# Kernel tuning notes

Measured on AMD Instinct MI355X. Metric: run time of the kernel, lower is better.

Reference implementation:

```python
import jax, jax.numpy as jnp
import numpy as np

TOP_K = 4
ALPHA = 1.702
LIMIT = 7.0


def _glu(x):
    # interleaved gate/up split, clamp, custom swiglu
    gate = x[..., ::2]
    up = x[..., 1::2]
    gate = jnp.minimum(gate, LIMIT)
    up = jnp.clip(up, -LIMIT, LIMIT)
    glu = gate * jax.nn.sigmoid(gate * ALPHA)
    return (up + 1.0) * glu


def setup_inputs() -> dict:
    key = jax.random.key(0)
    ks = jax.random.split(key, 7)
    B, S, H, F, E = 1, 1024, 2880, 2880, 16
    w_scale = 0.02
    return {
        "hidden_states": jax.random.normal(ks[0], (B, S, H), dtype=jnp.float32),
        "router_w": jax.random.normal(ks[1], (E, H), dtype=jnp.float32) * w_scale,
        "router_b": jax.random.normal(ks[2], (E,), dtype=jnp.float32) * w_scale,
        "gate_up_w": jax.random.normal(ks[3], (E, H, 2 * F), dtype=jnp.float32) * w_scale,
        "gate_up_b": jax.random.normal(ks[4], (E, 2 * F), dtype=jnp.float32) * w_scale,
        "down_w": jax.random.normal(ks[5], (E, F, H), dtype=jnp.float32) * w_scale,
        "down_b": jax.random.normal(ks[6], (E, H), dtype=jnp.float32) * w_scale,
    }


def reference(hidden_states, router_w, router_b, gate_up_w, gate_up_b, down_w, down_b):
    B, S, H = hidden_states.shape
    x = hidden_states.reshape(-1, H)  # [T, H]
    T = x.shape[0]

    # Router: linear + top-k + softmax over top-k values, scattered to full [T, E]
    logits = x @ router_w.T + router_b  # [T, E]
    top_v, top_i = jax.lax.top_k(logits, TOP_K)  # [T, K]
    top_v = jax.nn.softmax(top_v, axis=-1)  # normalized top-k affinities
    scores = jnp.zeros_like(logits).at[jnp.arange(T)[:, None], top_i].set(top_v)  # [T, E]

    # Expert GLU MLPs (dense over experts; zero affinity masks unselected experts)
    gu = jnp.einsum('th,ehf->etf', x, gate_up_w) + gate_up_b[:, None, :]  # [E, T, 2F]
    act = _glu(gu)  # [E, T, F]
    out_e = jnp.einsum('etf,efh->eth', act, down_w) + down_b[:, None, :]  # [E, T, H]

    # Combine weighted by router scores
    out = jnp.einsum('te,eth->th', scores, out_e)  # [T, H]
    return out.reshape(B, S, H)
```

## Files before the change

### kernel.cpp

```cpp
#include <hip/hip_runtime.h>
#include <hip/hip_bf16.h>
#include <math.h>

#define H_DIM 2880
#define F_DIM 2880
#define GU_DIM 5760
#define NE 16
#define NT 1024
#define TOPK 4

typedef float f32x4 __attribute__((ext_vector_type(4)));
typedef __bf16 bf16x8 __attribute__((ext_vector_type(8)));

__device__ __forceinline__ unsigned short f2bf(float f) {
    union { float f; unsigned u; } v; v.f = f;
    return (unsigned short)((v.u + 0x8000u) >> 16);
}
__device__ __forceinline__ unsigned pk2(float a, float b) {
    return (unsigned)f2bf(a) | ((unsigned)f2bf(b) << 16);
}
__device__ __forceinline__ void gload16(const void* gsrc, void* ldst) {
    __builtin_amdgcn_global_load_lds(
        (const __attribute__((address_space(1))) unsigned int*)gsrc,
        (__attribute__((address_space(3))) unsigned int*)ldst,
        16, 0, 0);
}

__global__ __launch_bounds__(256) void castx_kernel(const float* __restrict__ x,
                                                    unsigned short* __restrict__ xb)
{
    int i = (blockIdx.x * 256 + threadIdx.x) * 8;
    float4 a = *(const float4*)(x + i);
    float4 b = *(const float4*)(x + i + 4);
    uint4 o;
    o.x = pk2(a.x, a.y); o.y = pk2(a.z, a.w);
    o.z = pk2(b.x, b.y); o.w = pk2(b.z, b.w);
    *(uint4*)(xb + i) = o;
}

__global__ __launch_bounds__(64) void router_kernel(
    const float* __restrict__ x, const float* __restrict__ rw, const float* __restrict__ rb,
    int* counts, int* topk_idx, float* topk_score)
{
    int t = blockIdx.x, lane = threadIdx.x;
    const float* xr = x + (size_t)t * H_DIM;
    float acc[NE];
#pragma unroll
    for (int e = 0; e < NE; e++) acc[e] = 0.f;
    for (int h = lane; h < H_DIM; h += 64) {
        float xv = xr[h];
#pragma unroll
        for (int e = 0; e < NE; e++) acc[e] += xv * rw[e * H_DIM + h];
    }
    float lg[NE];
#pragma unroll
    for (int e = 0; e < NE; e++) {
        float v = acc[e];
#pragma unroll
        for (int off = 32; off > 0; off >>= 1) v += __shfl_down(v, off, 64);
        lg[e] = v;
    }
    if (lane == 0) {
#pragma unroll
        for (int e = 0; e < NE; e++) lg[e] += rb[e];
        int mask = 0; float tv[TOPK]; int ti[TOPK];
        for (int k = 0; k < TOPK; k++) {
            float best = -1e30f; int bi = 0;
            for (int e = 0; e < NE; e++)
                if (!((mask >> e) & 1) && lg[e] > best) { best = lg[e]; bi = e; }
            mask |= 1 << bi; tv[k] = best; ti[k] = bi;
        }
        float m = tv[0], s = 0.f, ex[TOPK];
        for (int k = 0; k < TOPK; k++) { ex[k] = expf(tv[k] - m); s += ex[k]; }
        float inv = 1.f / s;
        for (int k = 0; k < TOPK; k++) {
            topk_idx[t * TOPK + k] = ti[k];
            topk_score[t * TOPK + k] = ex[k] * inv;
            atomicAdd(&counts[ti[k]], 1);
        }
    }
}

__global__ void offsets_kernel(const int* counts, int* offsets) {
    if (threadIdx.x == 0 && blockIdx.x == 0) {
        int s = 0;
        for (int e = 0; e < NE; e++) { offsets[e] = s; s += counts[e]; }
        offsets[NE] = s;
    }
}

__global__ void scatter_kernel(const int* topk_idx, const float* topk_score,
                               const int* offsets, int* fills, int* entry, float* entry_score,
                               int* slot_map)
{
    int t = blockIdx.x * blockDim.x + threadIdx.x;
    if (t >= NT) return;
    for (int k = 0; k < TOPK; k++) {
        int e = topk_idx[t * TOPK + k];
        int pos = atomicAdd(&fills[e], 1);
        int i = offsets[e] + pos;
        entry[i] = t | (k << 16);
        entry_score[i] = topk_score[t * TOPK + k];
        slot_map[t * TOPK + k] = i;
    }
}

__global__ __launch_bounds__(256, 2) void gemm1_kernel(
    const unsigned short* __restrict__ xb, const float* __restrict__ gw, const float* __restrict__ gb,
    const int* __restrict__ counts, const int* __restrict__ offsets,
    const int* __restrict__ entry, unsigned short* __restrict__ act)
{
    int e = blockIdx.z;
    int cnt = counts[e];
    int m0 = blockIdx.y * 128;
    if (m0 >= cnt) return;
    int n0 = blockIdx.x * 128;
    int off = offsets[e];

    __shared__ __align__(16) unsigned short As[128 * 32];
    __shared__ __align__(16) unsigned short Bs[128 * 40];
    __shared__ int toks[128];

    int tid = threadIdx.x;
    if (tid < 128) {
        int r = m0 + tid;
        toks[tid] = entry[off + (r < cnt ? r : 0)] & 0xFFFF;
    }
    __syncthreads();

    int wv = tid >> 6, lane = tid & 63;

    int ar0 = 32 * wv + (lane >> 2);
    int ar1 = ar0 + 16;
    int ac = lane & 3;
    const unsigned short* asrc0 = xb + (size_t)toks[ar0] * H_DIM + 8 * (ac ^ ((ar0 >> 1) & 3));
    const unsigned short* asrc1 = xb + (size_t)toks[ar1] * H_DIM + 8 * (ac ^ ((ar1 >> 1) & 3));
    unsigned short* adst0 = &As[(32 * wv) * 32];
    unsigned short* adst1 = &As[(32 * wv + 16) * 32];

    int n4 = tid & 31, kb = tid >> 5;
    const float* bptr = gw + (size_t)e * H_DIM * GU_DIM + (size_t)kb * 4 * GU_DIM + n0 + n4 * 4;

    int wm = (wv & 1) * 64, wn = (wv >> 1) * 64;
    int r16 = lane & 15, q = lane >> 4;

    f32x4 acc[4][4] = {};
    int a_rd[4], b_rd[4];
#pragma unroll
    for (int i = 0; i < 4; i++) {
        int m = wm + i * 16 + r16;
        a_rd[i] = m * 32 + ((q ^ ((m >> 1) & 3)) * 8);
        int n = wn + i * 16 + r16;
        b_rd[i] = n * 40 + ((q ^ ((n >> 2) & 3)) * 8);
    }
    int bwr[4];
#pragma unroll
    for (int c = 0; c < 4; c++) {
        int nl = n4 * 4 + c;
        bwr[c] = nl * 40 + (((kb >> 1) ^ ((nl >> 2) & 3)) * 8) + (kb & 1) * 4;
    }

    for (int k0 = 0; k0 < H_DIM; k0 += 32) {
        gload16(asrc0 + k0, adst0);
        gload16(asrc1 + k0, adst1);
        float bvf[4][4];
#pragma unroll
        for (int j = 0; j < 4; j++) {
            float4 tv = *(const float4*)(bptr + (size_t)(k0 + j) * GU_DIM);
            bvf[j][0] = tv.x; bvf[j][1] = tv.y; bvf[j][2] = tv.z; bvf[j][3] = tv.w;
        }
#pragma unroll
        for (int c = 0; c < 4; c++)
            *(uint2*)&Bs[bwr[c]] = make_uint2(pk2(bvf[0][c], bvf[1][c]), pk2(bvf[2][c], bvf[3][c]));
        __syncthreads();

        bf16x8 af[4], bq[4];
#pragma unroll
        for (int i = 0; i < 4; i++) af[i] = *(const bf16x8*)&As[a_rd[i]];
#pragma unroll
        for (int i = 0; i < 4; i++) bq[i] = *(const bf16x8*)&Bs[b_rd[i]];
#pragma unroll
        for (int mi = 0; mi < 4; mi++)
#pragma unroll
            for (int ni = 0; ni < 4; ni++)
                acc[mi][ni] = __builtin_amdgcn_mfma_f32_16x16x32_bf16(af[mi], bq[ni], acc[mi][ni], 0, 0, 0);
        __syncthreads();
    }

    const float* gbp = gb + (size_t)e * GU_DIM;
#pragma unroll
    for (int ni = 0; ni < 4; ni++) {
        int col = n0 + wn + ni * 16 + r16;
        float bias = gbp[col];
#pragma unroll
        for (int mi = 0; mi < 4; mi++) {
#pragma unroll
            for (int r = 0; r < 4; r++) {
                float v = acc[mi][ni][r] + bias;
                float vo = __shfl_xor(v, 1, 64);
                float gate = (lane & 1) ? vo : v;
                float up   = (lane & 1) ? v  : vo;
                gate = fminf(gate, 7.0f);
                up = fminf(fmaxf(up, -7.0f), 7.0f);
                float glu = gate / (1.0f + expf(-1.702f * gate));
                float a = (up + 1.0f) * glu;
                int row = m0 + wm + mi * 16 + q * 4 + r;
                if (row < cnt && !(lane & 1))
                    act[(size_t)(off + row) * F_DIM + (col >> 1)] = f2bf(a);
            }
        }
    }
}

__global__ __launch_bounds__(256, 2) void gemm2_kernel(
    const unsigned short* __restrict__ act, const float* __restrict__ dw, const float* __restrict__ db,
    const int* __restrict__ counts, const int* __restrict__ offsets,
    const float* __restrict__ entry_score, float* __restrict__ slot_out)
{
    int e = blockIdx.z;
    int cnt = counts[e];
    int m0 = blockIdx.y * 128;
    if (m0 >= cnt) return;
    int n0 = blockIdx.x * 128;
    int off = offsets[e];

    __shared__ __align__(16) unsigned short As[128 * 32];
    __shared__ __align__(16) unsigned short Bs[128 * 40];
    __shared__ float scs[128];

    int tid = threadIdx.x;
    if (tid < 128) {
        int r = m0 + tid;
        scs[tid] = entry_score[off + (r < cnt ? r : 0)];
    }
    __syncthreads();

    int wv = tid >> 6, lane = tid & 63;

    int ar0 = 32 * wv + (lane >> 2);
    int ar1 = ar0 + 16;
    int ac = lane & 3;
    const unsigned short* asrc0 = act + (size_t)(off + m0 + ar0) * F_DIM + 8 * (ac ^ ((ar0 >> 1) & 3));
    const unsigned short* asrc1 = act + (size_t)(off + m0 + ar1) * F_DIM + 8 * (ac ^ ((ar1 >> 1) & 3));
    unsigned short* adst0 = &As[(32 * wv) * 32];
    unsigned short* adst1 = &As[(32 * wv + 16) * 32];

    int n4 = tid & 31, kb = tid >> 5;
    int ncol = n0 + n4 * 4;
    bool nval = ncol < H_DIM;
    const float* bptr = dw + (size_t)e * F_DIM * H_DIM + (size_t)kb * 4 * H_DIM + ncol;

    int wm = (wv & 1) * 64, wn = (wv >> 1) * 64;
    int r16 = lane & 15, q = lane >> 4;

    f32x4 acc[4][4] = {};
    int a_rd[4], b_rd[4];
#pragma unroll
    for (int i = 0; i < 4; i++) {
        int m = wm + i * 16 + r16;
        a_rd[i] = m * 32 + ((q ^ ((m >> 1) & 3)) * 8);
        int n = wn + i * 16 + r16;
        b_rd[i] = n * 40 + ((q ^ ((n >> 2) & 3)) * 8);
    }
    int bwr[4];
#pragma unroll
    for (int c = 0; c < 4; c++) {
        int nl = n4 * 4 + c;
        bwr[c] = nl * 40 + (((kb >> 1) ^ ((nl >> 2) & 3)) * 8) + (kb & 1) * 4;
    }

    for (int k0 = 0; k0 < F_DIM; k0 += 32) {
        gload16(asrc0 + k0, adst0);
        gload16(asrc1 + k0, adst1);
        float bvf[4][4];
#pragma unroll
        for (int j = 0; j < 4; j++) {
            float4 tv = nval ? *(const float4*)(bptr + (size_t)(k0 + j) * H_DIM)
                             : make_float4(0.f, 0.f, 0.f, 0.f);
            bvf[j][0] = tv.x; bvf[j][1] = tv.y; bvf[j][2] = tv.z; bvf[j][3] = tv.w;
        }
#pragma unroll
        for (int c = 0; c < 4; c++)
            *(uint2*)&Bs[bwr[c]] = make_uint2(pk2(bvf[0][c], bvf[1][c]), pk2(bvf[2][c], bvf[3][c]));
        __syncthreads();

        bf16x8 af[4], bq[4];
#pragma unroll
        for (int i = 0; i < 4; i++) af[i] = *(const bf16x8*)&As[a_rd[i]];
#pragma unroll
        for (int i = 0; i < 4; i++) bq[i] = *(const bf16x8*)&Bs[b_rd[i]];
#pragma unroll
        for (int mi = 0; mi < 4; mi++)
#pragma unroll
            for (int ni = 0; ni < 4; ni++)
                acc[mi][ni] = __builtin_amdgcn_mfma_f32_16x16x32_bf16(af[mi], bq[ni], acc[mi][ni], 0, 0, 0);
        __syncthreads();
    }

    const float* dbp = db + (size_t)e * H_DIM;
#pragma unroll
    for (int ni = 0; ni < 4; ni++) {
        int col = n0 + wn + ni * 16 + r16;
        float bias = (col < H_DIM) ? dbp[col] : 0.f;
#pragma unroll
        for (int mi = 0; mi < 4; mi++) {
#pragma unroll
            for (int r = 0; r < 4; r++) {
                int lr = wm + mi * 16 + q * 4 + r;
                if (m0 + lr < cnt && col < H_DIM) {
                    float v = (acc[mi][ni][r] + bias) * scs[lr];
                    slot_out[(size_t)(off + m0 + lr) * H_DIM + col] = v;
                }
            }
        }
    }
}

__global__ __launch_bounds__(256) void gather_kernel(
    const float* __restrict__ slot_out, const int* __restrict__ slot_map,
    float* __restrict__ out)
{
    int t = blockIdx.x;
    int s0 = slot_map[t * TOPK + 0];
    int s1 = slot_map[t * TOPK + 1];
    int s2 = slot_map[t * TOPK + 2];
    int s3 = slot_map[t * TOPK + 3];
    const float* r0 = slot_out + (size_t)s0 * H_DIM;
    const float* r1 = slot_out + (size_t)s1 * H_DIM;
    const float* r2 = slot_out + (size_t)s2 * H_DIM;
    const float* r3 = slot_out + (size_t)s3 * H_DIM;
    float* op = out + (size_t)t * H_DIM;
    for (int h = threadIdx.x * 4; h < H_DIM; h += 1024) {
        f32x4 v = *(const f32x4*)(r0 + h) + *(const f32x4*)(r1 + h)
                + *(const f32x4*)(r2 + h) + *(const f32x4*)(r3 + h);
        *(f32x4*)(op + h) = v;
    }
}

extern "C" void kernel_launch(void* const* d_in, const int* in_sizes, int n_in,
                              void* d_out, int out_size, void* d_ws, size_t ws_size,
                              hipStream_t stream)
{
    const float* x  = (const float*)d_in[0];
    const float* rw = (const float*)d_in[1];
    const float* rb = (const float*)d_in[2];
    const float* gw = (const float*)d_in[3];
    const float* gb = (const float*)d_in[4];
    const float* dw = (const float*)d_in[5];
    const float* db = (const float*)d_in[6];
    float* out = (float*)d_out;

    char* ws = (char*)d_ws;
    int*   counts      = (int*)(ws);
    int*   fills       = (int*)(ws + 64);
    int*   offsets     = (int*)(ws + 128);
    int*   topk_idx    = (int*)(ws + 256);
    float* topk_score  = (float*)(ws + 16640);
    int*   entry       = (int*)(ws + 33024);
    float* entry_score = (float*)(ws + 49408);
    int*   slot_map    = (int*)(ws + 65792);
    unsigned short* act = (unsigned short*)(ws + 131072);
    unsigned short* xb  = (unsigned short*)(ws + 131072 + 24330240);
    float* slot_out     = (float*)(ws + 30359552);

    hipMemsetAsync(ws, 0, 256, stream);

    castx_kernel<<<1440, 256, 0, stream>>>(x, xb);
    router_kernel<<<NT, 64, 0, stream>>>(x, rw, rb, counts, topk_idx, topk_score);
    offsets_kernel<<<1, 32, 0, stream>>>(counts, offsets);
    scatter_kernel<<<4, 256, 0, stream>>>(topk_idx, topk_score, offsets, fills, entry, entry_score, slot_map);
    gemm1_kernel<<<dim3(45, 8, NE), 256, 0, stream>>>(xb, gw, gb, counts, offsets, entry, act);
    gemm2_kernel<<<dim3(23, 8, NE), 256, 0, stream>>>(act, dw, db, counts, offsets, entry_score, slot_out);
    gather_kernel<<<NT, 256, 0, stream>>>(slot_out, slot_map, out);
}
```

Before: 2.142 ms.

## Double-buffer LDS and enlarge M tile to 256 rows in expert GEMMs

Both expert GEMM kernels now use 512-thread blocks covering 256 token rows, so each converted fp32 weight tile is reused across twice as many rows. LDS is double-buffered: the next A tile and the next weight loads are issued before the current MFMA step, and the weight tile is stored after it, leaving one barrier per iteration. This targets the heavy fp32 weight traffic and load latency, at the cost of more LDS, padded work for experts with few tokens, and fewer blocks in the grid. Workspace offsets are shifted so the act buffer has room for the larger padded row reads.

```diff
diff --git a/kernel.cpp b/kernel.cpp
--- a/kernel.cpp
+++ b/kernel.cpp
@@ -8,6 +8,7 @@
 #define NE 16
 #define NT 1024
 #define TOPK 4
+#define NIT (H_DIM / 32)
 
 typedef float f32x4 __attribute__((ext_vector_type(4)));
 typedef __bf16 bf16x8 __attribute__((ext_vector_type(8)));
@@ -105,24 +106,24 @@
     }
 }
 
-__global__ __launch_bounds__(256, 2) void gemm1_kernel(
+__global__ __launch_bounds__(512) void gemm1_kernel(
     const unsigned short* __restrict__ xb, const float* __restrict__ gw, const float* __restrict__ gb,
     const int* __restrict__ counts, const int* __restrict__ offsets,
     const int* __restrict__ entry, unsigned short* __restrict__ act)
 {
     int e = blockIdx.z;
     int cnt = counts[e];
-    int m0 = blockIdx.y * 128;
+    int m0 = blockIdx.y * 256;
     if (m0 >= cnt) return;
     int n0 = blockIdx.x * 128;
     int off = offsets[e];
 
-    __shared__ __align__(16) unsigned short As[128 * 32];
-    __shared__ __align__(16) unsigned short Bs[128 * 40];
-    __shared__ int toks[128];
+    __shared__ __align__(16) unsigned short As[2][256 * 32];
+    __shared__ __align__(16) unsigned short Bs[2][128 * 40];
+    __shared__ int toks[256];
 
     int tid = threadIdx.x;
-    if (tid < 128) {
+    if (tid < 256) {
         int r = m0 + tid;
         toks[tid] = entry[off + (r < cnt ? r : 0)] & 0xFFFF;
     }
@@ -135,13 +136,19 @@
     int ac = lane & 3;
     const unsigned short* asrc0 = xb + (size_t)toks[ar0] * H_DIM + 8 * (ac ^ ((ar0 >> 1) & 3));
     const unsigned short* asrc1 = xb + (size_t)toks[ar1] * H_DIM + 8 * (ac ^ ((ar1 >> 1) & 3));
-    unsigned short* adst0 = &As[(32 * wv) * 32];
-    unsigned short* adst1 = &As[(32 * wv + 16) * 32];
-
-    int n4 = tid & 31, kb = tid >> 5;
+    int aoff0 = (32 * wv) * 32;
+    int aoff1 = (32 * wv + 16) * 32;
+
+    int n4 = tid & 31, kb = (tid >> 5) & 7;
     const float* bptr = gw + (size_t)e * H_DIM * GU_DIM + (size_t)kb * 4 * GU_DIM + n0 + n4 * 4;
-
-    int wm = (wv & 1) * 64, wn = (wv >> 1) * 64;
+    int bwr[4];
+#pragma unroll
+    for (int c = 0; c < 4; c++) {
+        int nl = n4 * 4 + c;
+        bwr[c] = nl * 40 + (((kb >> 1) ^ ((nl >> 2) & 3)) * 8) + (kb & 1) * 4;
+    }
+
+    int wm = (wv >> 1) * 64, wn = (wv & 1) * 64;
     int r16 = lane & 15, q = lane >> 4;
 
     f32x4 acc[4][4] = {};
@@ -153,37 +160,53 @@
         int n = wn + i * 16 + r16;
         b_rd[i] = n * 40 + ((q ^ ((n >> 2) & 3)) * 8);
     }
-    int bwr[4];
-#pragma unroll
-    for (int c = 0; c < 4; c++) {
-        int nl = n4 * 4 + c;
-        bwr[c] = nl * 40 + (((kb >> 1) ^ ((nl >> 2) & 3)) * 8) + (kb & 1) * 4;
-    }
-
-    for (int k0 = 0; k0 < H_DIM; k0 += 32) {
-        gload16(asrc0 + k0, adst0);
-        gload16(asrc1 + k0, adst1);
+
+    gload16(asrc0, &As[0][aoff0]);
+    gload16(asrc1, &As[0][aoff1]);
+    if (tid < 256) {
         float bvf[4][4];
 #pragma unroll
         for (int j = 0; j < 4; j++) {
-            float4 tv = *(const float4*)(bptr + (size_t)(k0 + j) * GU_DIM);
+            float4 tv = *(const float4*)(bptr + (size_t)j * GU_DIM);
             bvf[j][0] = tv.x; bvf[j][1] = tv.y; bvf[j][2] = tv.z; bvf[j][3] = tv.w;
         }
 #pragma unroll
         for (int c = 0; c < 4; c++)
-            *(uint2*)&Bs[bwr[c]] = make_uint2(pk2(bvf[0][c], bvf[1][c]), pk2(bvf[2][c], bvf[3][c]));
-        __syncthreads();
-
+            *(uint2*)&Bs[0][bwr[c]] = make_uint2(pk2(bvf[0][c], bvf[1][c]), pk2(bvf[2][c], bvf[3][c]));
+    }
+    __syncthreads();
+
+    for (int it = 0; it < NIT; it++) {
+        int cur = it & 1, nxt = cur ^ 1;
+        int k1 = (it + 1) * 32;
+        bool more = (it + 1 < NIT);
+        float bvf[4][4];
+        if (more) {
+            gload16(asrc0 + k1, &As[nxt][aoff0]);
+            gload16(asrc1 + k1, &As[nxt][aoff1]);
+            if (tid < 256) {
+#pragma unroll
+                for (int j = 0; j < 4; j++) {
+                    float4 tv = *(const float4*)(bptr + (size_t)(k1 + j) * GU_DIM);
+                    bvf[j][0] = tv.x; bvf[j][1] = tv.y; bvf[j][2] = tv.z; bvf[j][3] = tv.w;
+                }
+            }
+        }
         bf16x8 af[4], bq[4];
 #pragma unroll
-        for (int i = 0; i < 4; i++) af[i] = *(const bf16x8*)&As[a_rd[i]];
-#pragma unroll
-        for (int i = 0; i < 4; i++) bq[i] = *(const bf16x8*)&Bs[b_rd[i]];
+        for (int i = 0; i < 4; i++) af[i] = *(const bf16x8*)&As[cur][a_rd[i]];
+#pragma unroll
+        for (int i = 0; i < 4; i++) bq[i] = *(const bf16x8*)&Bs[cur][b_rd[i]];
 #pragma unroll
         for (int mi = 0; mi < 4; mi++)
 #pragma unroll
             for (int ni = 0; ni < 4; ni++)
                 acc[mi][ni] = __builtin_amdgcn_mfma_f32_16x16x32_bf16(af[mi], bq[ni], acc[mi][ni], 0, 0, 0);
+        if (more && tid < 256) {
+#pragma unroll
+            for (int c = 0; c < 4; c++)
+                *(uint2*)&Bs[nxt][bwr[c]] = make_uint2(pk2(bvf[0][c], bvf[1][c]), pk2(bvf[2][c], bvf[3][c]));
+        }
         __syncthreads();
     }
 
@@ -212,24 +235,24 @@
     }
 }
 
-__global__ __launch_bounds__(256, 2) void gemm2_kernel(
+__global__ __launch_bounds__(512) void gemm2_kernel(
     const unsigned short* __restrict__ act, const float* __restrict__ dw, const float* __restrict__ db,
     const int* __restrict__ counts, const int* __restrict__ offsets,
     const float* __restrict__ entry_score, float* __restrict__ slot_out)
 {
     int e = blockIdx.z;
     int cnt = counts[e];
-    int m0 = blockIdx.y * 128;
+    int m0 = blockIdx.y * 256;
     if (m0 >= cnt) return;
     int n0 = blockIdx.x * 128;
     int off = offsets[e];
 
-    __shared__ __align__(16) unsigned short As[128 * 32];
-    __shared__ __align__(16) unsigned short Bs[128 * 40];
-    __shared__ float scs[128];
+    __shared__ __align__(16) unsigned short As[2][256 * 32];
+    __shared__ __align__(16) unsigned short Bs[2][128 * 40];
+    __shared__ float scs[256];
 
     int tid = threadIdx.x;
-    if (tid < 128) {
+    if (tid < 256) {
         int r = m0 + tid;
         scs[tid] = entry_score[off + (r < cnt ? r : 0)];
     }
@@ -242,15 +265,21 @@
     int ac = lane & 3;
     const unsigned short* asrc0 = act + (size_t)(off + m0 + ar0) * F_DIM + 8 * (ac ^ ((ar0 >> 1) & 3));
     const unsigned short* asrc1 = act + (size_t)(off + m0 + ar1) * F_DIM + 8 * (ac ^ ((ar1 >> 1) & 3));
-    unsigned short* adst0 = &As[(32 * wv) * 32];
-    unsigned short* adst1 = &As[(32 * wv + 16) * 32];
-
-    int n4 = tid & 31, kb = tid >> 5;
+    int aoff0 = (32 * wv) * 32;
+    int aoff1 = (32 * wv + 16) * 32;
+
+    int n4 = tid & 31, kb = (tid >> 5) & 7;
     int ncol = n0 + n4 * 4;
     bool nval = ncol < H_DIM;
     const float* bptr = dw + (size_t)e * F_DIM * H_DIM + (size_t)kb * 4 * H_DIM + ncol;
-
-    int wm = (wv & 1) * 64, wn = (wv >> 1) * 64;
+    int bwr[4];
+#pragma unroll
+    for (int c = 0; c < 4; c++) {
+        int nl = n4 * 4 + c;
+        bwr[c] = nl * 40 + (((kb >> 1) ^ ((nl >> 2) & 3)) * 8) + (kb & 1) * 4;
+    }
+
+    int wm = (wv >> 1) * 64, wn = (wv & 1) * 64;
     int r16 = lane & 15, q = lane >> 4;
 
     f32x4 acc[4][4] = {};
@@ -262,38 +291,55 @@
         int n = wn + i * 16 + r16;
         b_rd[i] = n * 40 + ((q ^ ((n >> 2) & 3)) * 8);
     }
-    int bwr[4];
-#pragma unroll
-    for (int c = 0; c < 4; c++) {
-        int nl = n4 * 4 + c;
-        bwr[c] = nl * 40 + (((kb >> 1) ^ ((nl >> 2) & 3)) * 8) + (kb & 1) * 4;
-    }
-
-    for (int k0 = 0; k0 < F_DIM; k0 += 32) {
-        gload16(asrc0 + k0, adst0);
-        gload16(asrc1 + k0, adst1);
+
+    gload16(asrc0, &As[0][aoff0]);
+    gload16(asrc1, &As[0][aoff1]);
+    if (tid < 256) {
         float bvf[4][4];
 #pragma unroll
         for (int j = 0; j < 4; j++) {
-            float4 tv = nval ? *(const float4*)(bptr + (size_t)(k0 + j) * H_DIM)
+            float4 tv = nval ? *(const float4*)(bptr + (size_t)j * H_DIM)
                              : make_float4(0.f, 0.f, 0.f, 0.f);
             bvf[j][0] = tv.x; bvf[j][1] = tv.y; bvf[j][2] = tv.z; bvf[j][3] = tv.w;
         }
 #pragma unroll
         for (int c = 0; c < 4; c++)
-            *(uint2*)&Bs[bwr[c]] = make_uint2(pk2(bvf[0][c], bvf[1][c]), pk2(bvf[2][c], bvf[3][c]));
-        __syncthreads();
-
+            *(uint2*)&Bs[0][bwr[c]] = make_uint2(pk2(bvf[0][c], bvf[1][c]), pk2(bvf[2][c], bvf[3][c]));
+    }
+    __syncthreads();
+
+    for (int it = 0; it < NIT; it++) {
+        int cur = it & 1, nxt = cur ^ 1;
+        int k1 = (it + 1) * 32;
+        bool more = (it + 1 < NIT);
+        float bvf[4][4];
+        if (more) {
+            gload16(asrc0 + k1, &As[nxt][aoff0]);
+            gload16(asrc1 + k1, &As[nxt][aoff1]);
+            if (tid < 256) {
+#pragma unroll
+                for (int j = 0; j < 4; j++) {
+                    float4 tv = nval ? *(const float4*)(bptr + (size_t)(k1 + j) * H_DIM)
+                                     : make_float4(0.f, 0.f, 0.f, 0.f);
+                    bvf[j][0] = tv.x; bvf[j][1] = tv.y; bvf[j][2] = tv.z; bvf[j][3] = tv.w;
+                }
+            }
+        }
         bf16x8 af[4], bq[4];
 #pragma unroll
-        for (int i = 0; i < 4; i++) af[i] = *(const bf16x8*)&As[a_rd[i]];
-#pragma unroll
-        for (int i = 0; i < 4; i++) bq[i] = *(const bf16x8*)&Bs[b_rd[i]];
+        for (int i = 0; i < 4; i++) af[i] = *(const bf16x8*)&As[cur][a_rd[i]];
+#pragma unroll
+        for (int i = 0; i < 4; i++) bq[i] = *(const bf16x8*)&Bs[cur][b_rd[i]];
 #pragma unroll
         for (int mi = 0; mi < 4; mi++)
 #pragma unroll
             for (int ni = 0; ni < 4; ni++)
                 acc[mi][ni] = __builtin_amdgcn_mfma_f32_16x16x32_bf16(af[mi], bq[ni], acc[mi][ni], 0, 0, 0);
+        if (more && tid < 256) {
+#pragma unroll
+            for (int c = 0; c < 4; c++)
+                *(uint2*)&Bs[nxt][bwr[c]] = make_uint2(pk2(bvf[0][c], bvf[1][c]), pk2(bvf[2][c], bvf[3][c]));
+        }
         __syncthreads();
     }
 
@@ -360,8 +406,8 @@
     float* entry_score = (float*)(ws + 49408);
     int*   slot_map    = (int*)(ws + 65792);
     unsigned short* act = (unsigned short*)(ws + 131072);
-    unsigned short* xb  = (unsigned short*)(ws + 131072 + 24330240);
-    float* slot_out     = (float*)(ws + 30359552);
+    unsigned short* xb  = (unsigned short*)(ws + 25198592);
+    float* slot_out     = (float*)(ws + 31096832);
 
     hipMemsetAsync(ws, 0, 256, stream);
 
@@ -369,7 +415,7 @@
     router_kernel<<<NT, 64, 0, stream>>>(x, rw, rb, counts, topk_idx, topk_score);
     offsets_kernel<<<1, 32, 0, stream>>>(counts, offsets);
     scatter_kernel<<<4, 256, 0, stream>>>(topk_idx, topk_score, offsets, fills, entry, entry_score, slot_map);
-    gemm1_kernel<<<dim3(45, 8, NE), 256, 0, stream>>>(xb, gw, gb, counts, offsets, entry, act);
-    gemm2_kernel<<<dim3(23, 8, NE), 256, 0, stream>>>(act, dw, db, counts, offsets, entry_score, slot_out);
+    gemm1_kernel<<<dim3(45, 4, NE), 512, 0, stream>>>(xb, gw, gb, counts, offsets, entry, act);
+    gemm2_kernel<<<dim3(23, 4, NE), 512, 0, stream>>>(act, dw, db, counts, offsets, entry_score, slot_out);
     gather_kernel<<<NT, 256, 0, stream>>>(slot_out, slot_map, out);
 }
```

Measured after the change: 2.097 ms. -2.1%, faster.

## Triple-buffer grouped GEMM loads and enlarge M tile to 256 rows

Applied to the files above, without the earlier changes.

Both expert GEMMs now use 512-thread blocks with 256-row M tiles and a three-stage LDS ring. Global loads for the A tile (direct to LDS) and the fp32 weight tile (staged in registers) are issued two iterations ahead, with explicit vmcnt waits and a single barrier per step. This aims to hide memory latency behind MFMA work and to halve how often each weight tile is re-read, since it is shared across more token rows. The cost is more LDS and register pressure, and wasted rows for experts with few tokens. The workspace layout shifts to leave room for padded activation rows.

```diff
diff --git a/kernel.cpp b/kernel.cpp
--- a/kernel.cpp
+++ b/kernel.cpp
@@ -8,6 +8,7 @@
 #define NE 16
 #define NT 1024
 #define TOPK 4
+#define NIT 90
 
 typedef float f32x4 __attribute__((ext_vector_type(4)));
 typedef __bf16 bf16x8 __attribute__((ext_vector_type(8)));
@@ -105,24 +106,75 @@
     }
 }
 
-__global__ __launch_bounds__(256, 2) void gemm1_kernel(
+
+#define PIPE_ISSUE(ASRC0, ASRC1, BPTR, BSTRIDE, KK, NB, RS)                   \
+    {                                                                         \
+        gload16((ASRC0) + (KK), &As[NB][aoff0]);                              \
+        gload16((ASRC1) + (KK), &As[NB][aoff1]);                              \
+        RS[0] = *(const float4*)((BPTR) + (size_t)(KK) * (BSTRIDE));          \
+        RS[1] = *(const float4*)((BPTR) + (size_t)((KK) + 1) * (BSTRIDE));    \
+        asm volatile("" ::: "memory");                                        \
+    }
+
+#define PIPE_BWRITE(NB, RC)                                                   \
+    {                                                                         \
+        float4 t0_ = RC[0], t1_ = RC[1];                                      \
+        *(unsigned*)&Bs[NB][bwr0] = pk2(t0_.x, t1_.x);                        \
+        *(unsigned*)&Bs[NB][bwr1] = pk2(t0_.y, t1_.y);                        \
+        *(unsigned*)&Bs[NB][bwr2] = pk2(t0_.z, t1_.z);                        \
+        *(unsigned*)&Bs[NB][bwr3] = pk2(t0_.w, t1_.w);                        \
+    }
+
+#define PIPE_BARRIER()                                                        \
+    asm volatile("s_waitcnt lgkmcnt(0)" ::: "memory");                        \
+    __builtin_amdgcn_sched_barrier(0);                                        \
+    __builtin_amdgcn_s_barrier();                                             \
+    __builtin_amdgcn_sched_barrier(0);
+
+#define PIPE_MFMA(CUR)                                                        \
+    {                                                                         \
+        bf16x8 af_[4], bq_[4];                                                \
+        _Pragma("unroll") for (int i = 0; i < 4; i++)                         \
+            af_[i] = *(const bf16x8*)&As[CUR][a_rd[i]];                       \
+        _Pragma("unroll") for (int i = 0; i < 4; i++)                         \
+            bq_[i] = *(const bf16x8*)&Bs[CUR][b_rd[i]];                       \
+        _Pragma("unroll") for (int mi = 0; mi < 4; mi++)                      \
+            _Pragma("unroll") for (int ni = 0; ni < 4; ni++)                  \
+                acc[mi][ni] = __builtin_amdgcn_mfma_f32_16x16x32_bf16(        \
+                    af_[mi], bq_[ni], acc[mi][ni], 0, 0, 0);                  \
+    }
+
+#define PIPE_BODY(ASRC0, ASRC1, BPTR, BSTRIDE, T, CUR, NB1, NB2, RISS, RCON)  \
+    {                                                                         \
+        bool more_ = (T) + 2 < NIT;                                           \
+        if (more_) PIPE_ISSUE(ASRC0, ASRC1, BPTR, BSTRIDE, ((T) + 2) * 32, NB2, RISS); \
+        PIPE_MFMA(CUR);                                                       \
+        if ((T) + 1 < NIT) {                                                  \
+            if (more_) { asm volatile("s_waitcnt vmcnt(4)" ::: "memory"); }   \
+            else       { asm volatile("s_waitcnt vmcnt(0)" ::: "memory"); }   \
+            PIPE_BWRITE(NB1, RCON);                                           \
+            PIPE_BARRIER();                                                   \
+        }                                                                     \
+    }
+
+__global__ __launch_bounds__(512, 4) void gemm1_kernel(
     const unsigned short* __restrict__ xb, const float* __restrict__ gw, const float* __restrict__ gb,
     const int* __restrict__ counts, const int* __restrict__ offsets,
     const int* __restrict__ entry, unsigned short* __restrict__ act)
 {
     int e = blockIdx.z;
     int cnt = counts[e];
-    int m0 = blockIdx.y * 128;
+    int m0 = blockIdx.y * 256;
     if (m0 >= cnt) return;
     int n0 = blockIdx.x * 128;
     int off = offsets[e];
 
-    __shared__ __align__(16) unsigned short As[128 * 32];
-    __shared__ __align__(16) unsigned short Bs[128 * 40];
-    __shared__ int toks[128];
+    __shared__ __align__(16) unsigned short As[3][256 * 32];
+    __shared__ __align__(16) unsigned short Bs[3][128 * 40];
+    __shared__ int toks[256];
 
     int tid = threadIdx.x;
-    if (tid < 128) {
+    if (tid < 256) {
         int r = m0 + tid;
         toks[tid] = entry[off + (r < cnt ? r : 0)] & 0xFFFF;
     }
@@ -135,13 +187,18 @@
     int ac = lane & 3;
     const unsigned short* asrc0 = xb + (size_t)toks[ar0] * H_DIM + 8 * (ac ^ ((ar0 >> 1) & 3));
     const unsigned short* asrc1 = xb + (size_t)toks[ar1] * H_DIM + 8 * (ac ^ ((ar1 >> 1) & 3));
-    unsigned short* adst0 = &As[(32 * wv) * 32];
-    unsigned short* adst1 = &As[(32 * wv + 16) * 32];
-
-    int n4 = tid & 31, kb = tid >> 5;
-    const float* bptr = gw + (size_t)e * H_DIM * GU_DIM + (size_t)kb * 4 * GU_DIM + n0 + n4 * 4;
-
-    int wm = (wv & 1) * 64, wn = (wv >> 1) * 64;
+    int aoff0 = (32 * wv) * 32;
+    int aoff1 = (32 * wv + 16) * 32;
+
+    int n4 = tid & 31, ks = tid >> 5;
+    const float* bptr = gw + (size_t)e * H_DIM * GU_DIM + (size_t)(ks * 2) * GU_DIM + n0 + n4 * 4;
+    int bswz = (((ks >> 2) ^ (n4 & 3)) * 8) + (ks & 3) * 2;
+    int bwr0 = (n4 * 4 + 0) * 40 + bswz;
+    int bwr1 = (n4 * 4 + 1) * 40 + bswz;
+    int bwr2 = (n4 * 4 + 2) * 40 + bswz;
+    int bwr3 = (n4 * 4 + 3) * 40 + bswz;
+
+    int wm = (wv >> 1) * 64, wn = (wv & 1) * 64;
     int r16 = lane & 15, q = lane >> 4;
 
     f32x4 acc[4][4] = {};
@@ -153,38 +210,21 @@
         int n = wn + i * 16 + r16;
         b_rd[i] = n * 40 + ((q ^ ((n >> 2) & 3)) * 8);
     }
-    int bwr[4];
-#pragma unroll
-    for (int c = 0; c < 4; c++) {
-        int nl = n4 * 4 + c;
-        bwr[c] = nl * 40 + (((kb >> 1) ^ ((nl >> 2) & 3)) * 8) + (kb & 1) * 4;
-    }
-
-    for (int k0 = 0; k0 < H_DIM; k0 += 32) {
-        gload16(asrc0 + k0, adst0);
-        gload16(asrc1 + k0, adst1);
-        float bvf[4][4];
-#pragma unroll
-        for (int j = 0; j < 4; j++) {
-            float4 tv = *(const float4*)(bptr + (size_t)(k0 + j) * GU_DIM);
-            bvf[j][0] = tv.x; bvf[j][1] = tv.y; bvf[j][2] = tv.z; bvf[j][3] = tv.w;
-        }
-#pragma unroll
-        for (int c = 0; c < 4; c++)
-            *(uint2*)&Bs[bwr[c]] = make_uint2(pk2(bvf[0][c], bvf[1][c]), pk2(bvf[2][c], bvf[3][c]));
-        __syncthreads();
-
-        bf16x8 af[4], bq[4];
-#pragma unroll
-        for (int i = 0; i < 4; i++) af[i] = *(const bf16x8*)&As[a_rd[i]];
-#pragma unroll
-        for (int i = 0; i < 4; i++) bq[i] = *(const bf16x8*)&Bs[b_rd[i]];
-#pragma unroll
-        for (int mi = 0; mi < 4; mi++)
-#pragma unroll
-            for (int ni = 0; ni < 4; ni++)
-                acc[mi][ni] = __builtin_amdgcn_mfma_f32_16x16x32_bf16(af[mi], bq[ni], acc[mi][ni], 0, 0, 0);
-        __syncthreads();
+
+    float4 rA[2], rB[2];
+    PIPE_ISSUE(asrc0, asrc1, bptr, GU_DIM, 0, 0, rA);
+    PIPE_ISSUE(asrc0, asrc1, bptr, GU_DIM, 32, 1, rB);
+    asm volatile("s_waitcnt vmcnt(4)" ::: "memory");
+    PIPE_BWRITE(0, rA);
+    PIPE_BARRIER();
+
+    int c0 = 0;
+    for (int it = 0; it < NIT; it += 2) {
+        int c1 = c0 + 1; if (c1 == 3) c1 = 0;
+        int c2 = c1 + 1; if (c2 == 3) c2 = 0;
+        PIPE_BODY(asrc0, asrc1, bptr, GU_DIM, it,     c0, c1, c2, rA, rB);
+        PIPE_BODY(asrc0, asrc1, bptr, GU_DIM, it + 1, c1, c2, c0, rB, rA);
+        c0 = c2;
     }
 
     const float* gbp = gb + (size_t)e * GU_DIM;
@@ -212,24 +252,24 @@
     }
 }
 
-__global__ __launch_bounds__(256, 2) void gemm2_kernel(
+__global__ __launch_bounds__(512, 4) void gemm2_kernel(
     const unsigned short* __restrict__ act, const float* __restrict__ dw, const float* __restrict__ db,
     const int* __restrict__ counts, const int* __restrict__ offsets,
     const float* __restrict__ entry_score, float* __restrict__ slot_out)
 {
     int e = blockIdx.z;
     int cnt = counts[e];
-    int m0 = blockIdx.y * 128;
+    int m0 = blockIdx.y * 256;
     if (m0 >= cnt) return;
     int n0 = blockIdx.x * 128;
     int off = offsets[e];
 
-    __shared__ __align__(16) unsigned short As[128 * 32];
-    __shared__ __align__(16) unsigned short Bs[128 * 40];
-    __shared__ float scs[128];
+    __shared__ __align__(16) unsigned short As[3][256 * 32];
+    __shared__ __align__(16) unsigned short Bs[3][128 * 40];
+    __shared__ float scs[256];
 
     int tid = threadIdx.x;
-    if (tid < 128) {
+    if (tid < 256) {
         int r = m0 + tid;
         scs[tid] = entry_score[off + (r < cnt ? r : 0)];
     }
@@ -242,15 +282,20 @@
     int ac = lane & 3;
     const unsigned short* asrc0 = act + (size_t)(off + m0 + ar0) * F_DIM + 8 * (ac ^ ((ar0 >> 1) & 3));
     const unsigned short* asrc1 = act + (size_t)(off + m0 + ar1) * F_DIM + 8 * (ac ^ ((ar1 >> 1) & 3));
-    unsigned short* adst0 = &As[(32 * wv) * 32];
-    unsigned short* adst1 = &As[(32 * wv + 16) * 32];
-
-    int n4 = tid & 31, kb = tid >> 5;
+    int aoff0 = (32 * wv) * 32;
+    int aoff1 = (32 * wv + 16) * 32;
+
+    int n4 = tid & 31, ks = tid >> 5;
     int ncol = n0 + n4 * 4;
-    bool nval = ncol < H_DIM;
-    const float* bptr = dw + (size_t)e * F_DIM * H_DIM + (size_t)kb * 4 * H_DIM + ncol;
-
-    int wm = (wv & 1) * 64, wn = (wv >> 1) * 64;
+    int ncc = (ncol < H_DIM) ? ncol : (H_DIM - 4);
+    const float* bptr = dw + (size_t)e * F_DIM * H_DIM + (size_t)(ks * 2) * H_DIM + ncc;
+    int bswz = (((ks >> 2) ^ (n4 & 3)) * 8) + (ks & 3) * 2;
+    int bwr0 = (n4 * 4 + 0) * 40 + bswz;
+    int bwr1 = (n4 * 4 + 1) * 40 + bswz;
+    int bwr2 = (n4 * 4 + 2) * 40 + bswz;
+    int bwr3 = (n4 * 4 + 3) * 40 + bswz;
+
+    int wm = (wv >> 1) * 64, wn = (wv & 1) * 64;
     int r16 = lane & 15, q = lane >> 4;
 
     f32x4 acc[4][4] = {};
@@ -262,39 +307,21 @@
         int n = wn + i * 16 + r16;
         b_rd[i] = n * 40 + ((q ^ ((n >> 2) & 3)) * 8);
     }
-    int bwr[4];
-#pragma unroll
-    for (int c = 0; c < 4; c++) {
-        int nl = n4 * 4 + c;
-        bwr[c] = nl * 40 + (((kb >> 1) ^ ((nl >> 2) & 3)) * 8) + (kb & 1) * 4;
-    }
-
-    for (int k0 = 0; k0 < F_DIM; k0 += 32) {
-        gload16(asrc0 + k0, adst0);
-        gload16(asrc1 + k0, adst1);
-        float bvf[4][4];
-#pragma unroll
-        for (int j = 0; j < 4; j++) {
-            float4 tv = nval ? *(const float4*)(bptr + (size_t)(k0 + j) * H_DIM)
-                             : make_float4(0.f, 0.f, 0.f, 0.f);
-            bvf[j][0] = tv.x; bvf[j][1] = tv.y; bvf[j][2] = tv.z; bvf[j][3] = tv.w;
-        }
-#pragma unroll
-        for (int c = 0; c < 4; c++)
-            *(uint2*)&Bs[bwr[c]] = make_uint2(pk2(bvf[0][c], bvf[1][c]), pk2(bvf[2][c], bvf[3][c]));
-        __syncthreads();
-
-        bf16x8 af[4], bq[4];
-#pragma unroll
-        for (int i = 0; i < 4; i++) af[i] = *(const bf16x8*)&As[a_rd[i]];
-#pragma unroll
-        for (int i = 0; i < 4; i++) bq[i] = *(const bf16x8*)&Bs[b_rd[i]];
-#pragma unroll
-        for (int mi = 0; mi < 4; mi++)
-#pragma unroll
-            for (int ni = 0; ni < 4; ni++)
-                acc[mi][ni] = __builtin_amdgcn_mfma_f32_16x16x32_bf16(af[mi], bq[ni], acc[mi][ni], 0, 0, 0);
-        __syncthreads();
+
+    float4 rA[2], rB[2];
+    PIPE_ISSUE(asrc0, asrc1, bptr, H_DIM, 0, 0, rA);
+    PIPE_ISSUE(asrc0, asrc1, bptr, H_DIM, 32, 1, rB);
+    asm volatile("s_waitcnt vmcnt(4)" ::: "memory");
+    PIPE_BWRITE(0, rA);
+    PIPE_BARRIER();
+
+    int c0 = 0;
+    for (int it = 0; it < NIT; it += 2) {
+        int c1 = c0 + 1; if (c1 == 3) c1 = 0;
+        int c2 = c1 + 1; if (c2 == 3) c2 = 0;
+        PIPE_BODY(asrc0, asrc1, bptr, H_DIM, it,     c0, c1, c2, rA, rB);
+        PIPE_BODY(asrc0, asrc1, bptr, H_DIM, it + 1, c1, c2, c0, rB, rA);
+        c0 = c2;
     }
 
     const float* dbp = db + (size_t)e * H_DIM;
@@ -360,8 +387,8 @@
     float* entry_score = (float*)(ws + 49408);
     int*   slot_map    = (int*)(ws + 65792);
     unsigned short* act = (unsigned short*)(ws + 131072);
-    unsigned short* xb  = (unsigned short*)(ws + 131072 + 24330240);
-    float* slot_out     = (float*)(ws + 30359552);
+    unsigned short* xb  = (unsigned short*)(ws + 25198592);
+    float* slot_out     = (float*)(ws + 31096832);
 
     hipMemsetAsync(ws, 0, 256, stream);
 
@@ -369,7 +396,7 @@
     router_kernel<<<NT, 64, 0, stream>>>(x, rw, rb, counts, topk_idx, topk_score);
     offsets_kernel<<<1, 32, 0, stream>>>(counts, offsets);
     scatter_kernel<<<4, 256, 0, stream>>>(topk_idx, topk_score, offsets, fills, entry, entry_score, slot_map);
-    gemm1_kernel<<<dim3(45, 8, NE), 256, 0, stream>>>(xb, gw, gb, counts, offsets, entry, act);
-    gemm2_kernel<<<dim3(23, 8, NE), 256, 0, stream>>>(act, dw, db, counts, offsets, entry_score, slot_out);
+    gemm1_kernel<<<dim3(45, 4, NE), 512, 0, stream>>>(xb, gw, gb, counts, offsets, entry, act);
+    gemm2_kernel<<<dim3(23, 4, NE), 512, 0, stream>>>(act, dw, db, counts, offsets, entry_score, slot_out);
     gather_kernel<<<NT, 256, 0, stream>>>(slot_out, slot_map, out);
 }
```

Result: no change. 2.126 ms (-0.7%).
